# Optimization experiments

Measured on AMD Instinct MI355X. Metric: run time of the kernel, lower is better.

The kernel has to match this reference:

```python
import jax, jax.numpy as jnp
import numpy as np
import math

N_HEADS = 12
ROPE_DIM = 64
BASE = 10000.0


def _rope_tables(seq_len, dim):
    inv_freq = 1.0 / (BASE ** (jnp.arange(0, dim, 2, dtype=jnp.float32) / dim))
    t = jnp.arange(seq_len, dtype=jnp.float32)
    freqs = jnp.outer(t, inv_freq)                      # [S, dim/2]
    emb = jnp.concatenate([freqs, freqs], axis=-1)      # [S, dim]
    # broadcast shape [1, S, 1, dim]
    return jnp.cos(emb)[None, :, None, :], jnp.sin(emb)[None, :, None, :]


def _rotate_half(x):
    x1, x2 = jnp.split(x, 2, axis=-1)
    return jnp.concatenate([-x2, x1], axis=-1)


def setup_inputs() -> dict:
    key = jax.random.key(0)
    ks = jax.random.split(key, 9)
    B, S, E = 2, 2048, 768
    s = 1.0 / math.sqrt(E)
    return {
        "x": jax.random.normal(ks[0], (B, S, E), jnp.float32),
        "Wq": jax.random.normal(ks[1], (E, E), jnp.float32) * s,
        "bq": jax.random.normal(ks[2], (E,), jnp.float32) * 0.02,
        "Wk": jax.random.normal(ks[3], (E, E), jnp.float32) * s,
        "bk": jax.random.normal(ks[4], (E,), jnp.float32) * 0.02,
        "Wv": jax.random.normal(ks[5], (E, E), jnp.float32) * s,
        "bv": jax.random.normal(ks[6], (E,), jnp.float32) * 0.02,
        "Wp": jax.random.normal(ks[7], (E, E), jnp.float32) * s,
        "bp": jax.random.normal(ks[8], (E,), jnp.float32) * 0.02,
    }


def reference(x, Wq, bq, Wk, bk, Wv, bv, Wp, bp):
    B, S, E = x.shape
    H = N_HEADS
    D = E // H

    q = (x @ Wq + bq).reshape(B, S, H, D)
    k = (x @ Wk + bk).reshape(B, S, H, D)
    v = (x @ Wv + bv).reshape(B, S, H, D)

    # rotary on first ROPE_DIM dims (here ROPE_DIM == D, so full rotary)
    cos, sin = _rope_tables(S, ROPE_DIM)
    q_rot, q_pass = q[..., :ROPE_DIM], q[..., ROPE_DIM:]
    k_rot, k_pass = k[..., :ROPE_DIM], k[..., ROPE_DIM:]
    q_rot = q_rot * cos + _rotate_half(q_rot) * sin
    k_rot = k_rot * cos + _rotate_half(k_rot) * sin
    q = jnp.concatenate([q_rot, q_pass], axis=-1)
    k = jnp.concatenate([k_rot, k_pass], axis=-1)

    # scores [B, M, N, H]; mask before scaling (as in the torch code; -inf unchanged)
    att = jnp.einsum("bmhd,bnhd->bmnh", q, k)
    causal = jnp.tril(jnp.ones((S, S), dtype=bool))[None, :, :, None]
    att = jnp.where(causal, att, -jnp.inf)
    att = jax.nn.softmax(att / math.sqrt(D), axis=2)
    out = jnp.einsum("bmnh,bnhd->bmhd", att, v)

    return out.reshape(B, S, E) @ Wp + bp
```

## Files before the change

### kernel.cpp

```cpp
#include <hip/hip_runtime.h>
#include <stdint.h>

#define S_LEN 2048
#define EMB   768
#define NH    12
#define DH    64
#define M_TOT 4096
#define WELEM 589824
#define QELEM 3145728

typedef float  floatx4  __attribute__((ext_vector_type(4)));
typedef float  floatx16 __attribute__((ext_vector_type(16)));
typedef __bf16 bf16x8  __attribute__((ext_vector_type(8)));
typedef __bf16 bf16x4  __attribute__((ext_vector_type(4)));
typedef unsigned short ushortx4 __attribute__((ext_vector_type(4)));

__device__ __forceinline__ unsigned short f2bf(float f) {
    union { float f; unsigned u; } v; v.f = f;
    unsigned u = v.u;
    unsigned r = (u + 0x7FFFu + ((u >> 16) & 1u)) >> 16;
    return (unsigned short)r;
}

__device__ __forceinline__ void gl_lds16(const void* g, void* l) {
    __builtin_amdgcn_global_load_lds(
        (__attribute__((address_space(1))) const void*)g,
        (__attribute__((address_space(3))) void*)l, 16, 0, 0);
}

__global__ void cvt_all_kernel(const float* __restrict__ x, unsigned short* __restrict__ xb,
                               const float* __restrict__ W0, const float* __restrict__ W1,
                               const float* __restrict__ W2, const float* __restrict__ W3,
                               unsigned short* __restrict__ WT_all, float2* __restrict__ rope) {
    __shared__ float t[64][65];
    const int blk = blockIdx.x;
    if (blk < 3072) {
        int i = (blk * 256 + threadIdx.x) * 4;
        float4 v = *(const float4*)(x + i);
        ushortx4 r = { f2bf(v.x), f2bf(v.y), f2bf(v.z), f2bf(v.w) };
        *(ushortx4*)(xb + i) = r;
        return;
    }
    if (blk >= 3648) {
        int idx = (blk - 3648) * 256 + threadIdx.x;
        int s = idx >> 5, d = idx & 31;
        float f = exp2f((float)d * -0.41524101186092034f);
        float th = (float)s * f;
        float sn, cs; sincosf(th, &sn, &cs);
        rope[idx] = make_float2(cs, sn);
        return;
    }
    const int tc = blk - 3072;
    const int z = tc / 144, rr0 = tc % 144;
    const float* W = (z == 0) ? W0 : (z == 1 ? W1 : (z == 2 ? W2 : W3));
    unsigned short* O = WT_all + (size_t)z * WELEM;
    const int k0 = (rr0 % 12) * 64, n0 = (rr0 / 12) * 64;
    const int c = threadIdx.x & 63, r4 = threadIdx.x >> 6;
#pragma unroll
    for (int rr = 0; rr < 64; rr += 4) {
        int r = rr + r4;
        t[r][c] = W[(size_t)(k0 + r) * EMB + n0 + c];
    }
    __syncthreads();
#pragma unroll
    for (int rr = 0; rr < 64; rr += 4) {
        int nn = rr + r4;
        O[(size_t)(n0 + nn) * EMB + k0 + c] = f2bf(t[c][nn]);
    }
}

static __device__ __forceinline__ void gemm_core_128x128(
    const unsigned short* __restrict__ A, const unsigned short* __restrict__ BT,
    int m0, int n0, int K, int tid, floatx4 (&acc)[4][4],
    unsigned short* Als, unsigned short* Bls)
{
    const int lane = tid & 63;
    const int c0 = lane & 15, quad = lane >> 4;
    const int wave = tid >> 6;
    const int wm = (wave >> 1) * 64, wn = (wave & 1) * 64;

    for (int k0 = 0; k0 < K; k0 += 64) {
        __syncthreads();
#pragma unroll
        for (int it = 0; it < 4; ++it) {
            int ch = it * 256 + tid;
            int row = ch >> 3, sc = ch & 7;
            int cc = sc ^ (row & 7);
            gl_lds16(A  + (size_t)(m0 + row) * K + k0 + cc * 8, Als + ch * 8);
            gl_lds16(BT + (size_t)(n0 + row) * K + k0 + cc * 8, Bls + ch * 8);
        }
        __syncthreads();
        bf16x8 af[4][2], bfv[4][2];
#pragma unroll
        for (int ii = 0; ii < 4; ++ii) {
            int row = wm + 16 * ii + c0;
#pragma unroll
            for (int h = 0; h < 2; ++h)
                af[ii][h] = *(const bf16x8*)(Als + row * 64 + (((4 * h + quad) ^ (row & 7)) * 8));
        }
#pragma unroll
        for (int jj = 0; jj < 4; ++jj) {
            int row = wn + 16 * jj + c0;
#pragma unroll
            for (int h = 0; h < 2; ++h)
                bfv[jj][h] = *(const bf16x8*)(Bls + row * 64 + (((4 * h + quad) ^ (row & 7)) * 8));
        }
#pragma unroll
        for (int ii = 0; ii < 4; ++ii)
#pragma unroll
            for (int jj = 0; jj < 4; ++jj) {
                acc[ii][jj] = __builtin_amdgcn_mfma_f32_16x16x32_bf16(af[ii][0], bfv[jj][0], acc[ii][jj], 0, 0, 0);
                acc[ii][jj] = __builtin_amdgcn_mfma_f32_16x16x32_bf16(af[ii][1], bfv[jj][1], acc[ii][jj], 0, 0, 0);
            }
    }
}

__global__ __launch_bounds__(256, 3) void qkv_kernel(
    const unsigned short* __restrict__ xb, const unsigned short* __restrict__ WT_all,
    const float* __restrict__ bq, const float* __restrict__ bk, const float* __restrict__ bv,
    const float2* __restrict__ rope, unsigned short* __restrict__ qkv_out)
{
    __shared__ __align__(16) unsigned short Als[128 * 64];
    __shared__ __align__(16) unsigned short Bls[128 * 64];
    const int z = blockIdx.z;
    const float* bias = (z == 0) ? bq : (z == 1 ? bk : bv);
    __bf16* Cout = (__bf16*)(qkv_out + (size_t)z * QELEM);
    const int m0 = blockIdx.x * 128, n0 = blockIdx.y * 128;
    const int tid = threadIdx.x, lane = tid & 63, c0 = lane & 15, quad = lane >> 4, wave = tid >> 6;
    const int wm = (wave >> 1) * 64, wn = (wave & 1) * 64;

    floatx4 acc[4][4] = {};
    gemm_core_128x128(xb, WT_all + (size_t)z * WELEM, m0, n0, EMB, tid, acc, Als, Bls);

    if (z == 2) {
#pragma unroll
        for (int ii = 0; ii < 4; ++ii) {
            int m = m0 + wm + 16 * ii + quad * 4;
            int b = m >> 11, s = m & (S_LEN - 1);
#pragma unroll
            for (int jj = 0; jj < 4; ++jj) {
                int n = n0 + wn + 16 * jj + c0;
                int h = n >> 6, d = n & 63;
                float bn = bias[n];
                bf16x4 pv;
#pragma unroll
                for (int r = 0; r < 4; ++r) pv[r] = (__bf16)(acc[ii][jj][r] + bn);
                *(bf16x4*)(Cout + ((size_t)(b * NH + h) * DH + d) * S_LEN + s) = pv;
            }
        }
        return;
    }

#pragma unroll
    for (int ii = 0; ii < 4; ++ii) {
#pragma unroll
        for (int r = 0; r < 4; ++r) {
            int m = m0 + wm + 16 * ii + quad * 4 + r;
            int b = m >> 11, s = m & (S_LEN - 1);
            float vals[4];
#pragma unroll
            for (int jj = 0; jj < 4; ++jj) vals[jj] = acc[ii][jj][r] + bias[n0 + wn + 16 * jj + c0];
#pragma unroll
            for (int jj = 0; jj < 2; ++jj) {
                int d = 16 * jj + c0;
                float2 t = rope[s * 32 + d];
                float lo = vals[jj], hi = vals[jj + 2];
                vals[jj]     = lo * t.x - hi * t.y;
                vals[jj + 2] = hi * t.x + lo * t.y;
            }
            if (z == 0) {
#pragma unroll
                for (int jj = 0; jj < 4; ++jj) vals[jj] *= 0.18033688011112042f;
            }
#pragma unroll
            for (int jj = 0; jj < 4; ++jj) {
                int n = n0 + wn + 16 * jj + c0;
                int h = n >> 6, d = n & 63;
                Cout[((size_t)(b * NH + h) * S_LEN + s) * DH + d] = (__bf16)vals[jj];
            }
        }
    }
}

__global__ __launch_bounds__(256, 3) void flash_kernel(
    const unsigned short* __restrict__ Qg, const unsigned short* __restrict__ Kg,
    const unsigned short* __restrict__ Vt, unsigned short* __restrict__ Og)
{
    __shared__ __align__(16) unsigned short Kls[3][64 * 64];
    __shared__ __align__(16) unsigned short Vls[3][64 * 64];
    __shared__ float lred[2][64];

    const int i = blockIdx.x;
    const int kk = i >> 8, g = i & 255;
    const int r0 = (kk == 0) ? g : (kk == 1 ? 511 - g : 512 + g);
    const int qt = 31 - r0 / 24;
    const int bh = r0 % 24;
    const int b = bh / NH, h = bh % NH;
    const int m0 = qt * 64;
    const int tid = threadIdx.x, lane = tid & 63, wave = tid >> 6;
    const int wm2 = wave >> 1, wn2 = wave & 1;
    const int lr = lane & 31, hf = lane >> 5;
    const size_t base = (size_t)bh * S_LEN * DH;
    const int mrow = m0 + wm2 * 32 + lr;

    bf16x8 qf[4];
#pragma unroll
    for (int t = 0; t < 4; ++t)
        qf[t] = *(const bf16x8*)(Qg + base + (size_t)mrow * DH + 16 * t + 8 * hf);
    asm volatile("" :: "v"(qf[0]), "v"(qf[1]), "v"(qf[2]), "v"(qf[3]));

    floatx16 oa0 = {}, oa1 = {};
    float l_lane = 0.f;
    const float C = 23.083120654223414f;
    const int ntiles = qt + 1;

#define STAGE_TILE(T, BUF)                                                              \
    {                                                                                   \
        _Pragma("unroll")                                                               \
        for (int it = 0; it < 2; ++it) {                                                \
            int ch = it * 256 + tid;                                                    \
            int row = ch >> 3, cc = (ch & 7) ^ (row & 7);                               \
            gl_lds16(Kg + base + (size_t)((T) * 64 + row) * DH + cc * 8,                \
                     &Kls[BUF][ch * 8]);                                                \
            gl_lds16(Vt + base + (size_t)row * S_LEN + (T) * 64 + cc * 8,               \
                     &Vls[BUF][ch * 8]);                                                \
        }                                                                               \
    }

    STAGE_TILE(0, 0);
    if (ntiles > 1) STAGE_TILE(1, 1);

    for (int nt = 0; nt < ntiles; ++nt) {
        const int buf = nt % 3;
        if (nt + 1 < ntiles) asm volatile("s_waitcnt vmcnt(4)" ::: "memory");
        else                 asm volatile("s_waitcnt vmcnt(0)" ::: "memory");
        __builtin_amdgcn_s_barrier();
        asm volatile("" ::: "memory");
        if (nt + 2 < ntiles) STAGE_TILE(nt + 2, (nt + 2) % 3);
        const unsigned short* Kb = Kls[buf];
        const unsigned short* Vb = Vls[buf];

        floatx16 sa = {};
        __builtin_amdgcn_s_setprio(1);
#pragma unroll
        for (int t = 0; t < 4; ++t) {
            int row = wn2 * 32 + lr;
            int ck = (2 * t + hf) ^ (row & 7);
            bf16x8 kf = *(const bf16x8*)(Kb + row * 64 + ck * 8);
            sa = __builtin_amdgcn_mfma_f32_32x32x16_bf16(kf, qf[t], sa, 0, 0, 0);
        }
        __builtin_amdgcn_s_setprio(0);

        if (nt == ntiles - 1) {
#pragma unroll
            for (int r = 0; r < 16; ++r) {
                int n = nt * 64 + wn2 * 32 + (r & 3) + 8 * (r >> 2) + 4 * hf;
                if (n > mrow) sa[r] = -1e30f;
            }
        }

        unsigned W[8];
#pragma unroll
        for (int q = 0; q < 8; ++q) {
            float p0 = __builtin_amdgcn_exp2f(sa[2 * q] - C);
            float p1 = __builtin_amdgcn_exp2f(sa[2 * q + 1] - C);
            l_lane += p0 + p1;
            union { __bf16 bb[2]; unsigned u; } w;
            w.bb[0] = (__bf16)p0; w.bb[1] = (__bf16)p1;
            W[q] = w.u;
        }
        bf16x8 pb[2];
#pragma unroll
        for (int t2 = 0; t2 < 2; ++t2) {
            unsigned own0 = hf ? W[4 * t2 + 2] : W[4 * t2 + 0];
            unsigned own1 = hf ? W[4 * t2 + 3] : W[4 * t2 + 1];
            unsigned giv0 = hf ? W[4 * t2 + 0] : W[4 * t2 + 2];
            unsigned giv1 = hf ? W[4 * t2 + 1] : W[4 * t2 + 3];
            unsigned s0 = (unsigned)__shfl_xor((int)giv0, 32, 64);
            unsigned s1 = (unsigned)__shfl_xor((int)giv1, 32, 64);
            union { unsigned u[4]; bf16x8 v; } pk;
            pk.u[0] = hf ? s0 : own0;
            pk.u[1] = hf ? s1 : own1;
            pk.u[2] = hf ? own0 : s0;
            pk.u[3] = hf ? own1 : s1;
            pb[t2] = pk.v;
        }

        __builtin_amdgcn_s_setprio(1);
#pragma unroll
        for (int dt = 0; dt < 2; ++dt) {
            int d = 32 * dt + lr;
#pragma unroll
            for (int t2 = 0; t2 < 2; ++t2) {
                int cv = (wn2 * 4 + 2 * t2 + hf) ^ (d & 7);
                bf16x8 vf = *(const bf16x8*)(Vb + d * 64 + cv * 8);
                if (dt == 0) oa0 = __builtin_amdgcn_mfma_f32_32x32x16_bf16(vf, pb[t2], oa0, 0, 0, 0);
                else         oa1 = __builtin_amdgcn_mfma_f32_32x32x16_bf16(vf, pb[t2], oa1, 0, 0, 0);
            }
        }
        __builtin_amdgcn_s_setprio(0);
    }
#undef STAGE_TILE

    l_lane += __shfl_xor(l_lane, 32, 64);

    __syncthreads();
    float* red = (float*)&Kls[0][0];
    if (wn2 == 1) {
#pragma unroll
        for (int e = 0; e < 16; ++e) red[(wm2 * 32 + e) * 64 + lane]        = oa0[e];
#pragma unroll
        for (int e = 0; e < 16; ++e) red[(wm2 * 32 + 16 + e) * 64 + lane]   = oa1[e];
        lred[wm2][lane] = l_lane;
    }
    __syncthreads();
    if (wn2 == 0) {
        const float lt = l_lane + lred[wm2][lane];
        const float rl = 1.0f / lt;
        __bf16* Ob16 = (__bf16*)Og;
#pragma unroll
        for (int rg = 0; rg < 4; ++rg) {
            bf16x4 ov0, ov1;
#pragma unroll
            for (int j = 0; j < 4; ++j) {
                int e = rg * 4 + j;
                ov0[j] = (__bf16)((oa0[e] + red[(wm2 * 32 + e) * 64 + lane]) * rl);
                ov1[j] = (__bf16)((oa1[e] + red[(wm2 * 32 + 16 + e) * 64 + lane]) * rl);
            }
            int d = 8 * rg + 4 * hf;
            *(bf16x4*)(Ob16 + ((size_t)(b * S_LEN + mrow)) * EMB + h * DH + d)      = ov0;
            *(bf16x4*)(Ob16 + ((size_t)(b * S_LEN + mrow)) * EMB + h * DH + 32 + d) = ov1;
        }
    }
}

__global__ __launch_bounds__(256, 3) void proj_kernel(
    const unsigned short* __restrict__ Ob, const unsigned short* __restrict__ WpT,
    const float* __restrict__ bp, float* __restrict__ out)
{
    __shared__ __align__(16) unsigned short Als[128 * 64];
    __shared__ __align__(16) unsigned short Bls[128 * 64];
    const int m0 = blockIdx.x * 128, n0 = blockIdx.y * 128;
    const int tid = threadIdx.x, lane = tid & 63, c0 = lane & 15, quad = lane >> 4, wave = tid >> 6;
    const int wm = (wave >> 1) * 64, wn = (wave & 1) * 64;

    floatx4 acc[4][4] = {};
    gemm_core_128x128(Ob, WpT, m0, n0, EMB, tid, acc, Als, Bls);

#pragma unroll
    for (int ii = 0; ii < 4; ++ii)
#pragma unroll
        for (int r = 0; r < 4; ++r) {
            int m = m0 + wm + 16 * ii + quad * 4 + r;
#pragma unroll
            for (int jj = 0; jj < 4; ++jj) {
                int n = n0 + wn + 16 * jj + c0;
                out[(size_t)m * EMB + n] = acc[ii][jj][r] + bp[n];
            }
        }
}

extern "C" void kernel_launch(void* const* d_in, const int* in_sizes, int n_in,
                              void* d_out, int out_size, void* d_ws, size_t ws_size,
                              hipStream_t stream)
{
    (void)in_sizes; (void)n_in; (void)out_size;
    const float* x  = (const float*)d_in[0];
    const float* Wq = (const float*)d_in[1];
    const float* bq = (const float*)d_in[2];
    const float* Wk = (const float*)d_in[3];
    const float* bk = (const float*)d_in[4];
    const float* Wv = (const float*)d_in[5];
    const float* bv = (const float*)d_in[6];
    const float* Wp = (const float*)d_in[7];
    const float* bp = (const float*)d_in[8];

    unsigned short* ws  = (unsigned short*)d_ws;
    unsigned short* xb  = ws;
    unsigned short* WT  = xb + (size_t)QELEM;
    unsigned short* QKV = WT + 4 * (size_t)WELEM;
    unsigned short* Ob  = QKV + 3 * (size_t)QELEM;
    float2* rope = (float2*)(Ob + (size_t)QELEM);
    if (ws_size < ((size_t)QELEM * 5 + 4 * (size_t)WELEM) * 2 + 2048 * 32 * 8) return;

    cvt_all_kernel<<<3904, 256, 0, stream>>>(x, xb, Wq, Wk, Wv, Wp, WT, rope);
    qkv_kernel<<<dim3(32, 6, 3), 256, 0, stream>>>(xb, WT, bq, bk, bv, (const float2*)rope, QKV);
    flash_kernel<<<dim3(768), 256, 0, stream>>>(QKV, QKV + QELEM, QKV + 2 * (size_t)QELEM, Ob);
    proj_kernel<<<dim3(32, 6), 256, 0, stream>>>(Ob, WT + 3 * (size_t)WELEM, bp, (float*)d_out);
}
```

Measured before the change: 156.1 us.

## Split causal flash attention along KV into chunks with a separate combine kernel

Splits each query tile's KV range into chunks of up to 8 tiles, giving 1920 balanced work items instead of 768 uneven ones. Each chunk writes unnormalized fp32 partial outputs and row sums, and a new combine kernel adds them and normalizes to bf16. This relies on the fixed-max exp2 scheme, so partials can be summed directly without rescaling. The aim is to cut the load imbalance and tail of the causal workload, at the cost of about 32 MB of extra fp32 partial traffic and one more kernel launch.

```diff
diff --git a/kernel.cpp b/kernel.cpp
--- a/kernel.cpp
+++ b/kernel.cpp
@@ -8,6 +8,8 @@
 #define M_TOT 4096
 #define WELEM 589824
 #define QELEM 3145728
+#define NCHUNK 80
+#define NPART (24 * NCHUNK)
 
 typedef float  floatx4  __attribute__((ext_vector_type(4)));
 typedef float  floatx16 __attribute__((ext_vector_type(16)));
@@ -182,20 +184,23 @@
     }
 }
 
-__global__ __launch_bounds__(256, 3) void flash_kernel(
+__global__ __launch_bounds__(256, 3) void flash_partial_kernel(
     const unsigned short* __restrict__ Qg, const unsigned short* __restrict__ Kg,
-    const unsigned short* __restrict__ Vt, unsigned short* __restrict__ Og)
+    const unsigned short* __restrict__ Vt, float* __restrict__ Opart, float* __restrict__ lpart)
 {
     __shared__ __align__(16) unsigned short Kls[3][64 * 64];
     __shared__ __align__(16) unsigned short Vls[3][64 * 64];
     __shared__ float lred[2][64];
 
-    const int i = blockIdx.x;
-    const int kk = i >> 8, g = i & 255;
-    const int r0 = (kk == 0) ? g : (kk == 1 ? 511 - g : 512 + g);
-    const int qt = 31 - r0 / 24;
-    const int bh = r0 % 24;
-    const int b = bh / NH, h = bh % NH;
+    const int bx = blockIdx.x;
+    const int bh = bx / NCHUNK, ci = bx % NCHUNK;
+    int qt, c;
+    if (ci < 8)       { qt = ci;                 c = 0; }
+    else if (ci < 24) { qt = 8  + (ci - 8) / 2;  c = (ci - 8) % 2; }
+    else if (ci < 48) { qt = 16 + (ci - 24) / 3; c = (ci - 24) % 3; }
+    else              { qt = 24 + (ci - 48) / 4; c = (ci - 48) % 4; }
+    const int nt0 = c * 8;
+    const int ntend = (nt0 + 8 < qt + 1) ? nt0 + 8 : qt + 1;
     const int m0 = qt * 64;
     const int tid = threadIdx.x, lane = tid & 63, wave = tid >> 6;
     const int wm2 = wave >> 1, wn2 = wave & 1;
@@ -212,7 +217,6 @@
     floatx16 oa0 = {}, oa1 = {};
     float l_lane = 0.f;
     const float C = 23.083120654223414f;
-    const int ntiles = qt + 1;
 
 #define STAGE_TILE(T, BUF)                                                              \
     {                                                                                   \
@@ -227,16 +231,16 @@
         }                                                                               \
     }
 
-    STAGE_TILE(0, 0);
-    if (ntiles > 1) STAGE_TILE(1, 1);
-
-    for (int nt = 0; nt < ntiles; ++nt) {
-        const int buf = nt % 3;
-        if (nt + 1 < ntiles) asm volatile("s_waitcnt vmcnt(4)" ::: "memory");
-        else                 asm volatile("s_waitcnt vmcnt(0)" ::: "memory");
+    STAGE_TILE(nt0, 0);
+    if (nt0 + 1 < ntend) STAGE_TILE(nt0 + 1, 1);
+
+    for (int nt = nt0; nt < ntend; ++nt) {
+        const int buf = (nt - nt0) % 3;
+        if (nt + 1 < ntend) asm volatile("s_waitcnt vmcnt(4)" ::: "memory");
+        else                asm volatile("s_waitcnt vmcnt(0)" ::: "memory");
         __builtin_amdgcn_s_barrier();
         asm volatile("" ::: "memory");
-        if (nt + 2 < ntiles) STAGE_TILE(nt + 2, (nt + 2) % 3);
+        if (nt + 2 < ntend) STAGE_TILE(nt + 2, (nt + 2 - nt0) % 3);
         const unsigned short* Kb = Kls[buf];
         const unsigned short* Vb = Vls[buf];
 
@@ -251,7 +255,7 @@
         }
         __builtin_amdgcn_s_setprio(0);
 
-        if (nt == ntiles - 1) {
+        if (nt == qt) {
 #pragma unroll
             for (int r = 0; r < 16; ++r) {
                 int n = nt * 64 + wn2 * 32 + (r & 3) + 8 * (r >> 2) + 4 * hf;
@@ -316,21 +320,55 @@
     __syncthreads();
     if (wn2 == 0) {
         const float lt = l_lane + lred[wm2][lane];
-        const float rl = 1.0f / lt;
-        __bf16* Ob16 = (__bf16*)Og;
+        float* op = Opart + (size_t)bx * 4096;
 #pragma unroll
         for (int rg = 0; rg < 4; ++rg) {
-            bf16x4 ov0, ov1;
+            floatx4 v0, v1;
 #pragma unroll
             for (int j = 0; j < 4; ++j) {
                 int e = rg * 4 + j;
-                ov0[j] = (__bf16)((oa0[e] + red[(wm2 * 32 + e) * 64 + lane]) * rl);
-                ov1[j] = (__bf16)((oa1[e] + red[(wm2 * 32 + 16 + e) * 64 + lane]) * rl);
-            }
-            int d = 8 * rg + 4 * hf;
-            *(bf16x4*)(Ob16 + ((size_t)(b * S_LEN + mrow)) * EMB + h * DH + d)      = ov0;
-            *(bf16x4*)(Ob16 + ((size_t)(b * S_LEN + mrow)) * EMB + h * DH + 32 + d) = ov1;
-        }
+                v0[j] = oa0[e] + red[(wm2 * 32 + e) * 64 + lane];
+                v1[j] = oa1[e] + red[(wm2 * 32 + 16 + e) * 64 + lane];
+            }
+            int m = wm2 * 32 + lr, d0 = 8 * rg + 4 * hf;
+            *(floatx4*)(op + m * 64 + d0)      = v0;
+            *(floatx4*)(op + m * 64 + 32 + d0) = v1;
+        }
+        if (hf == 0) lpart[(size_t)bx * 64 + wm2 * 32 + lr] = lt;
+    }
+}
+
+__global__ __launch_bounds__(256, 4) void combine_kernel(
+    const float* __restrict__ Opart, const float* __restrict__ lpart,
+    unsigned short* __restrict__ Og)
+{
+    const int qt = blockIdx.x, bh = blockIdx.y;
+    const int b = bh / NH, h = bh % NH;
+    const int nc = (qt >> 3) + 1;
+    const int cb = (qt < 8) ? qt
+                 : (qt < 16) ? 8 + (qt - 8) * 2
+                 : (qt < 24) ? 24 + (qt - 16) * 3
+                 : 48 + (qt - 24) * 4;
+    const int pbase = bh * NCHUNK + cb;
+    const int t = threadIdx.x;
+    __bf16* Ob16 = (__bf16*)Og;
+#pragma unroll
+    for (int v = 0; v < 4; ++v) {
+        int idx = v * 256 + t;
+        int m = idx >> 4, d = (idx & 15) * 4;
+        floatx4 s = {};
+        float ls = 0.f;
+        for (int cc = 0; cc < nc; ++cc) {
+            const float* P = Opart + (size_t)(pbase + cc) * 4096;
+            floatx4 u = *(const floatx4*)(P + m * 64 + d);
+            s.x += u.x; s.y += u.y; s.z += u.z; s.w += u.w;
+            ls += lpart[(size_t)(pbase + cc) * 64 + m];
+        }
+        const float rl = 1.0f / ls;
+        bf16x4 o;
+        o[0] = (__bf16)(s.x * rl); o[1] = (__bf16)(s.y * rl);
+        o[2] = (__bf16)(s.z * rl); o[3] = (__bf16)(s.w * rl);
+        *(bf16x4*)(Ob16 + ((size_t)(b * S_LEN + qt * 64 + m)) * EMB + h * DH + d) = o;
     }
 }
 
@@ -380,11 +418,17 @@
     unsigned short* WT  = xb + (size_t)QELEM;
     unsigned short* QKV = WT + 4 * (size_t)WELEM;
     unsigned short* Ob  = QKV + 3 * (size_t)QELEM;
-    float2* rope = (float2*)(Ob + (size_t)QELEM);
-    if (ws_size < ((size_t)QELEM * 5 + 4 * (size_t)WELEM) * 2 + 2048 * 32 * 8) return;
+    float2* rope  = (float2*)(Ob + (size_t)QELEM);
+    float*  opart = (float*)(rope + 2048 * 32);
+    float*  lpart = opart + (size_t)NPART * 4096;
+    size_t need = ((size_t)QELEM * 5 + 4 * (size_t)WELEM) * 2 + (size_t)2048 * 32 * 8
+                + (size_t)NPART * 4096 * 4 + (size_t)NPART * 64 * 4;
+    if (ws_size < need) return;
 
     cvt_all_kernel<<<3904, 256, 0, stream>>>(x, xb, Wq, Wk, Wv, Wp, WT, rope);
     qkv_kernel<<<dim3(32, 6, 3), 256, 0, stream>>>(xb, WT, bq, bk, bv, (const float2*)rope, QKV);
-    flash_kernel<<<dim3(768), 256, 0, stream>>>(QKV, QKV + QELEM, QKV + 2 * (size_t)QELEM, Ob);
+    flash_partial_kernel<<<dim3(NPART), 256, 0, stream>>>(QKV, QKV + QELEM, QKV + 2 * (size_t)QELEM,
+                                                          opart, lpart);
+    combine_kernel<<<dim3(32, 24), 256, 0, stream>>>(opart, lpart, Ob);
     proj_kernel<<<dim3(32, 6), 256, 0, stream>>>(Ob, WT + 3 * (size_t)WELEM, bp, (float*)d_out);
 }
```

Result: slower. 164.4 us (+5.3%).
